# Performance work log

Hardware: AMD Instinct MI355X
Metric: run time of the kernel (lower is better)

## Reference

```python
import jax, jax.numpy as jnp
import numpy as np

N_NODES = 50000
N_EDGES = 600000
D = 128
N_LAYERS = 4  # 2 base + 2 resnet layers
N_GRAPHS = 64
NEG_SLOPE = 0.01  # F.leaky_relu default


def setup_inputs() -> dict:
    key = jax.random.key(0)
    k1, k2, k3, k4, k5 = jax.random.split(key, 5)
    x = jax.random.normal(k1, (N_NODES, D), dtype=jnp.float32)
    edge_index = jax.random.randint(k2, (2, N_EDGES), 0, N_NODES, dtype=jnp.int64)
    batch = jnp.sort(jax.random.randint(k3, (N_NODES,), 0, N_GRAPHS, dtype=jnp.int64))
    Wl = jax.random.normal(k4, (N_LAYERS, D, D), dtype=jnp.float32) * 0.05
    bl = jnp.zeros((N_LAYERS, D), dtype=jnp.float32)
    Wr = jax.random.normal(k5, (N_LAYERS, D, D), dtype=jnp.float32) * 0.05
    return {"x": x, "edge_index": edge_index, "batch": batch,
            "Wl": Wl, "bl": bl, "Wr": Wr}


def _mean_aggregate(x, src, dst, n_nodes):
    # mean over incoming neighbors; isolated nodes get 0 (PyG scatter-mean semantics)
    s = jax.ops.segment_sum(x[src], dst, num_segments=n_nodes)  # [N, D]
    cnt = jax.ops.segment_sum(jnp.ones((src.shape[0],), x.dtype), dst,
                              num_segments=n_nodes)
    return s / jnp.maximum(cnt, 1.0)[:, None]


def reference(x, edge_index, batch, Wl, bl, Wr):
    src, dst = edge_index[0], edge_index[1]
    n = x.shape[0]
    for i in range(N_LAYERS):
        agg = _mean_aggregate(x, src, dst, n)                      # [N, D]
        # SAGEConv: lin_l(agg) + lin_r(x); lin_l has bias, lin_r does not
        x_new = agg @ Wl[i].T + bl[i] + x @ Wr[i].T
        x_new = jnp.where(x_new >= 0, x_new, NEG_SLOPE * x_new)    # leaky_relu
        x = x_new if i < 2 else x + x_new                          # residual after first 2
    # global mean pool per graph
    pooled = jax.ops.segment_sum(x, batch, num_segments=N_GRAPHS)  # [G, D]
    counts = jax.ops.segment_sum(jnp.ones((n,), x.dtype), batch,
                                 num_segments=N_GRAPHS)
    return pooled / jnp.maximum(counts, 1.0)[:, None]
```

## Files before the change

kernel.cpp:

```cpp
#include <hip/hip_runtime.h>

#define N_NODES 50000
#define N_EDGES 600000
#define DIM 128
#define N_LAYERS 4
#define N_GRAPHS 64
#define NEG_SLOPE 0.01f
#define NB_SCAN ((N_NODES + 255) / 256)
#define RS 264

typedef __attribute__((ext_vector_type(8))) short short8;
typedef __attribute__((ext_vector_type(16))) float floatx16;

__device__ __forceinline__ unsigned short f2bf(float f) {
    union { float f; unsigned u; } c; c.f = f;
    unsigned u = c.u;
    unsigned r = (u + 0x7FFFu + ((u >> 16) & 1u)) >> 16;
    return (unsigned short)r;
}
__device__ __forceinline__ float bfraw2f(unsigned short b) {
    union { unsigned u; float f; } c; c.u = ((unsigned)b) << 16;
    return c.f;
}
__device__ __forceinline__ float bflo(unsigned u) {
    union { unsigned u; float f; } c; c.u = u << 16; return c.f;
}
__device__ __forceinline__ float bfhi(unsigned u) {
    union { unsigned u; float f; } c; c.u = u & 0xFFFF0000u; return c.f;
}


__global__ void zero_ints(int* p, int n) {
    int i = blockIdx.x * blockDim.x + threadIdx.x;
    if (i < n) p[i] = 0;
}

__global__ void convert_x(const float4* __restrict__ x, uint4* __restrict__ xb) {
    int i = blockIdx.x * blockDim.x + threadIdx.x;
    if (i >= N_NODES * DIM / 8) return;
    float4 a = x[i * 2], b = x[i * 2 + 1];
    uint4 o;
    o.x = ((unsigned)f2bf(a.y) << 16) | f2bf(a.x);
    o.y = ((unsigned)f2bf(a.w) << 16) | f2bf(a.z);
    o.z = ((unsigned)f2bf(b.y) << 16) | f2bf(b.x);
    o.w = ((unsigned)f2bf(b.w) << 16) | f2bf(b.z);
    xb[i] = o;
}

__global__ void pack_w(const float* __restrict__ Wl, const float* __restrict__ Wr,
                       ushort* __restrict__ wpk) {
    int s = blockIdx.x >> 2, t = blockIdx.x & 3;
    int m = blockIdx.y, layer = blockIdx.z;
    int l = threadIdx.x;
    const float* W = ((m == 0) ? Wl : Wr) + (size_t)layer * DIM * DIM;
    int n = t * 32 + (l & 31);
    int kb = s * 16 + (l >> 5) * 8;
    size_t off = ((((size_t)(layer * 2 + m) * 8 + s) * 4 + t) * 64 + l) * 8;
    for (int j = 0; j < 8; j++)
        wpk[off + j] = f2bf(W[n * DIM + kb + j]);
}

__global__ void count_deg(const int* __restrict__ dst, int* deg) {
    int e = blockIdx.x * blockDim.x + threadIdx.x;
    if (e < N_EDGES) atomicAdd(&deg[dst[e]], 1);
}

__global__ void scan_pass1(const int* __restrict__ deg, int* __restrict__ bsum) {
    int i = blockIdx.x * 256 + threadIdx.x;
    int v = (i < N_NODES) ? deg[i] : 0;
    for (int off = 32; off > 0; off >>= 1) v += __shfl_down(v, off, 64);
    __shared__ int ws[4];
    int lane = threadIdx.x & 63, w = threadIdx.x >> 6;
    if (lane == 0) ws[w] = v;
    __syncthreads();
    if (threadIdx.x == 0) bsum[blockIdx.x] = ws[0] + ws[1] + ws[2] + ws[3];
}

__global__ void scan_pass2(int* __restrict__ bsum) {
    __shared__ int sm[256];
    int t = threadIdx.x;
    int v = (t < NB_SCAN) ? bsum[t] : 0;
    sm[t] = v;
    __syncthreads();
    for (int off = 1; off < 256; off <<= 1) {
        int u = (t >= off) ? sm[t - off] : 0;
        __syncthreads();
        sm[t] += u;
        __syncthreads();
    }
    if (t < NB_SCAN) bsum[t] = sm[t] - v;
}

__global__ void scan_pass3(const int* __restrict__ deg, const int* __restrict__ bsum,
                           int* __restrict__ rp) {
    int i = blockIdx.x * 256 + threadIdx.x;
    int v = (i < N_NODES) ? deg[i] : 0;
    int lane = threadIdx.x & 63, w = threadIdx.x >> 6;
    int s = v;
    for (int off = 1; off < 64; off <<= 1) {
        int t = __shfl_up(s, off, 64);
        if (lane >= off) s += t;
    }
    __shared__ int ws[4];
    if (lane == 63) ws[w] = s;
    __syncthreads();
    int wo = 0;
    for (int k = 0; k < 4; k++) wo += (k < w) ? ws[k] : 0;
    int incl = s + wo + bsum[blockIdx.x];
    if (i < N_NODES) rp[i + 1] = incl;
    if (i == 0) rp[0] = 0;
}

__global__ void fill_csr(const int* __restrict__ src, const int* __restrict__ dst,
                         const int* __restrict__ rp, int* __restrict__ fill,
                         int* __restrict__ csr) {
    int e = blockIdx.x * blockDim.x + threadIdx.x;
    if (e >= N_EDGES) return;
    int d = dst[e];
    int pos = atomicAdd(&fill[d], 1);
    csr[rp[d] + pos] = src[e];
}

__global__ void graph_start(const int* __restrict__ batch, int* __restrict__ gstart) {
    int i = blockIdx.x * blockDim.x + threadIdx.x;
    if (i >= N_NODES) return;
    int b = batch[i];
    if (i == 0) {
        for (int g = 0; g <= b; g++) gstart[g] = 0;
    } else {
        int p = batch[i - 1];
        for (int g = p + 1; g <= b; g++) gstart[g] = i;
    }
    if (i == N_NODES - 1) {
        for (int g = b + 1; g <= N_GRAPHS; g++) gstart[g] = N_NODES;
    }
}

__global__ __launch_bounds__(256) void agg_mean_wave(const uint* __restrict__ x32,
                                                     const int* __restrict__ rp,
                                                     const int* __restrict__ csr,
                                                     uint* __restrict__ agg32) {
    int wv = threadIdx.x >> 6, lane = threadIdx.x & 63;
    int node = blockIdx.x * 4 + wv;
    if (node >= N_NODES) return;
    int s = rp[node], e = rp[node + 1];
    float a0 = 0.f, a1 = 0.f;
    for (int base = s; base < e; base += 64) {
        int cnt = min(64, e - base);
        unsigned myidx = (base + lane < e) ? (unsigned)csr[base + lane] : 0u;
        for (int j = 0; j < cnt; j += 8) {
            int c2 = min(8, cnt - j);
            unsigned v[8];
#pragma unroll
            for (int k = 0; k < 8; k++) {
                unsigned idx = __shfl(myidx, j + k, 64);
                v[k] = (k < c2) ? x32[(size_t)idx * 64 + lane] : 0u;
            }
#pragma unroll
            for (int k = 0; k < 8; k++) { a0 += bflo(v[k]); a1 += bfhi(v[k]); }
        }
    }
    float inv = 1.0f / (float)max(e - s, 1);
    unsigned o = ((unsigned)f2bf(a1 * inv) << 16) | f2bf(a0 * inv);
    agg32[(size_t)node * 64 + lane] = o;
}

__global__ __launch_bounds__(256) void fused_layer_mfma(const ushort* __restrict__ agg,
                                                        const ushort* __restrict__ xin,
                                                        ushort* __restrict__ xout,
                                                        const ushort* __restrict__ wpk,
                                                        const float* __restrict__ bias,
                                                        int residual) {
    __shared__ ushort sA[128 * RS];
    int t = threadIdx.x;
    int node0 = blockIdx.x * 128;

    const uint4* aggv = (const uint4*)(agg + (size_t)node0 * DIM);
    const uint4* xv   = (const uint4*)(xin + (size_t)node0 * DIM);
    for (int i = t; i < 128 * 32; i += 256) {
        int r = i >> 5, c = i & 31;
        uint4 val = make_uint4(0u, 0u, 0u, 0u);
        if (node0 + r < N_NODES)
            val = (c < 16) ? aggv[r * 16 + c] : xv[r * 16 + (c - 16)];
        *(uint4*)&sA[r * RS + c * 8] = val;
    }
    __syncthreads();

    int wv = t >> 6, l = t & 63;
    int m0 = wv * 32;
    const ushort* arow = &sA[(m0 + (l & 31)) * RS];
    int khalf = (l >> 5) * 8;

    floatx16 acc0, acc1, acc2, acc3;
    for (int ii = 0; ii < 16; ii++) acc0[ii] = acc1[ii] = acc2[ii] = acc3[ii] = 0.f;

    const ushort* wl8 = wpk + (size_t)l * 8;
#pragma unroll
    for (int s2 = 0; s2 < 16; s2++) {
        int m = s2 >> 3, s = s2 & 7;
        short8 a = *(const short8*)(arow + m * 128 + s * 16 + khalf);
        size_t fb = (size_t)((m * 8 + s) * 4) * 512;
        short8 b0 = *(const short8*)(wl8 + fb);
        short8 b1 = *(const short8*)(wl8 + fb + 512);
        short8 b2 = *(const short8*)(wl8 + fb + 1024);
        short8 b3 = *(const short8*)(wl8 + fb + 1536);
        acc0 = __builtin_amdgcn_mfma_f32_32x32x16_bf16(a, b0, acc0, 0, 0, 0);
        acc1 = __builtin_amdgcn_mfma_f32_32x32x16_bf16(a, b1, acc1, 0, 0, 0);
        acc2 = __builtin_amdgcn_mfma_f32_32x32x16_bf16(a, b2, acc2, 0, 0, 0);
        acc3 = __builtin_amdgcn_mfma_f32_32x32x16_bf16(a, b3, acc3, 0, 0, 0);
    }

    int col = l & 31;
    int rbase = 4 * (l >> 5);
    floatx16 accs[4] = {acc0, acc1, acc2, acc3};
    for (int t4 = 0; t4 < 4; t4++) {
        int n = t4 * 32 + col;
        float bv = bias[n];
#pragma unroll
        for (int r = 0; r < 16; r++) {
            int row = (r & 3) + 8 * (r >> 2) + rbase;
            int gm = m0 + row;
            int gn = node0 + gm;
            if (gn >= N_NODES) continue;
            float v = accs[t4][r] + bv;
            v = (v >= 0.f) ? v : NEG_SLOPE * v;
            if (residual) v += bfraw2f(sA[gm * RS + 128 + n]);
            xout[(size_t)gn * DIM + n] = f2bf(v);
        }
    }
}

__global__ __launch_bounds__(128) void pool_partial(const ushort* __restrict__ xb,
                                                    const int* __restrict__ batch,
                                                    float* __restrict__ pooled) {
    int nb = blockIdx.x * 128;
    int ne = min(nb + 128, N_NODES);
    int d = threadIdx.x;
    int gcur = batch[nb];
    float acc = 0.f;
    for (int n = nb; n < ne; n++) {
        int g = batch[n];
        if (g != gcur) {
            atomicAdd(&pooled[gcur * DIM + d], acc);
            acc = 0.f;
            gcur = g;
        }
        acc += bfraw2f(xb[(size_t)n * DIM + d]);
    }
    atomicAdd(&pooled[gcur * DIM + d], acc);
}

__global__ void pool_final(const float* __restrict__ pooled,
                           const int* __restrict__ gstart,
                           float* __restrict__ out) {
    int i = blockIdx.x * blockDim.x + threadIdx.x;
    if (i >= N_GRAPHS * DIM) return;
    int g = i >> 7;
    int cnt = gstart[g + 1] - gstart[g];
    out[i] = pooled[i] / (float)max(cnt, 1);
}


extern "C" void kernel_launch(void* const* d_in, const int* in_sizes, int n_in,
                              void* d_out, int out_size, void* d_ws, size_t ws_size,
                              hipStream_t stream) {
    const float* x     = (const float*)d_in[0];
    const int*   ei    = (const int*)d_in[1];
    const int*   batch = (const int*)d_in[2];
    const float* Wl    = (const float*)d_in[3];
    const float* bl    = (const float*)d_in[4];
    const float* Wr    = (const float*)d_in[5];
    float* out = (float*)d_out;

    const int* esrc = ei;
    const int* edst = ei + N_EDGES;

    ushort* xb0  = (ushort*)d_ws;
    ushort* xbuf = xb0 + (size_t)N_NODES * DIM;
    ushort* agg  = xbuf + (size_t)N_NODES * DIM;
    ushort* wpk  = agg + (size_t)N_NODES * DIM;
    int* deg    = (int*)(wpk + (size_t)N_LAYERS * 2 * DIM * DIM);
    int* fill   = deg + N_NODES;
    int* csr    = fill + N_NODES;
    int* rp     = csr + N_EDGES;
    int* gstart = rp + (N_NODES + 1);
    int* bsum   = gstart + (N_GRAPHS + 1);
    float* pooled = (float*)(bsum + NB_SCAN);

    zero_ints<<<(2 * N_NODES + 255) / 256, 256, 0, stream>>>(deg, 2 * N_NODES);
    zero_ints<<<(N_GRAPHS * DIM + 255) / 256, 256, 0, stream>>>((int*)pooled, N_GRAPHS * DIM);

    convert_x<<<(N_NODES * DIM / 8 + 255) / 256, 256, 0, stream>>>((const float4*)x, (uint4*)xb0);
    pack_w<<<dim3(32, 2, 4), 64, 0, stream>>>(Wl, Wr, wpk);
    count_deg<<<(N_EDGES + 255) / 256, 256, 0, stream>>>(edst, deg);

    scan_pass1<<<NB_SCAN, 256, 0, stream>>>(deg, bsum);
    scan_pass2<<<1, 256, 0, stream>>>(bsum);
    scan_pass3<<<NB_SCAN, 256, 0, stream>>>(deg, bsum, rp);

    fill_csr<<<(N_EDGES + 255) / 256, 256, 0, stream>>>(esrc, edst, rp, fill, csr);
    graph_start<<<(N_NODES + 255) / 256, 256, 0, stream>>>(batch, gstart);

    int agg_blocks = (N_NODES + 3) / 4;
    int gemm_blocks = (N_NODES + 127) / 128;
    for (int l = 0; l < N_LAYERS; l++) {
        const ushort* xin = (l == 0) ? xb0 : xbuf;
        agg_mean_wave<<<agg_blocks, 256, 0, stream>>>((const uint*)xin, rp, csr, (uint*)agg);
        fused_layer_mfma<<<gemm_blocks, 256, 0, stream>>>(
            agg, xin, xbuf, wpk + (size_t)l * 2 * DIM * DIM,
            bl + (size_t)l * DIM, (l >= 2) ? 1 : 0);
    }

    pool_partial<<<(N_NODES + 127) / 128, 128, 0, stream>>>(xbuf, batch, pooled);
    pool_final<<<(N_GRAPHS * DIM + 255) / 256, 256, 0, stream>>>(pooled, gstart, out);
}
```

Baseline: 375.0 us.

## Fuse neighbor mean aggregation into the per-layer MFMA GEMM kernel

The separate gather/mean kernel is merged into the layer kernel. Each wave now aggregates neighbors for its own 32 rows, two nodes at a time with 16-byte loads, and writes the bf16 means straight into shared memory before the MFMA GEMM. This removes the global write and re-read of the aggregation buffer and one launch per layer. Because neighbors are now read while outputs are written, the node features ping-pong between two buffers. The cost is that the latency-bound gather now runs on only a few hundred large-LDS blocks with few outstanding loads per wave, which may hide memory latency much worse than the old many-block gather kernel.

```diff
diff --git a/kernel.cpp b/kernel.cpp
--- a/kernel.cpp
+++ b/kernel.cpp
@@ -136,65 +136,92 @@
     }
 }
 
-__global__ __launch_bounds__(256) void agg_mean_wave(const uint* __restrict__ x32,
-                                                     const int* __restrict__ rp,
-                                                     const int* __restrict__ csr,
-                                                     uint* __restrict__ agg32) {
-    int wv = threadIdx.x >> 6, lane = threadIdx.x & 63;
-    int node = blockIdx.x * 4 + wv;
-    if (node >= N_NODES) return;
-    int s = rp[node], e = rp[node + 1];
-    float a0 = 0.f, a1 = 0.f;
-    for (int base = s; base < e; base += 64) {
-        int cnt = min(64, e - base);
-        unsigned myidx = (base + lane < e) ? (unsigned)csr[base + lane] : 0u;
-        for (int j = 0; j < cnt; j += 8) {
-            int c2 = min(8, cnt - j);
-            unsigned v[8];
-#pragma unroll
-            for (int k = 0; k < 8; k++) {
-                unsigned idx = __shfl(myidx, j + k, 64);
-                v[k] = (k < c2) ? x32[(size_t)idx * 64 + lane] : 0u;
-            }
-#pragma unroll
-            for (int k = 0; k < 8; k++) { a0 += bflo(v[k]); a1 += bfhi(v[k]); }
-        }
-    }
-    float inv = 1.0f / (float)max(e - s, 1);
-    unsigned o = ((unsigned)f2bf(a1 * inv) << 16) | f2bf(a0 * inv);
-    agg32[(size_t)node * 64 + lane] = o;
-}
-
-__global__ __launch_bounds__(256) void fused_layer_mfma(const ushort* __restrict__ agg,
-                                                        const ushort* __restrict__ xin,
-                                                        ushort* __restrict__ xout,
-                                                        const ushort* __restrict__ wpk,
-                                                        const float* __restrict__ bias,
-                                                        int residual) {
+__global__ __launch_bounds__(256) void sage_layer(const uint* __restrict__ x32,
+                                                  ushort* __restrict__ xout,
+                                                  const int* __restrict__ rp,
+                                                  const int* __restrict__ csr,
+                                                  const ushort* __restrict__ wpk,
+                                                  const float* __restrict__ bias,
+                                                  int residual) {
     __shared__ ushort sA[128 * RS];
     int t = threadIdx.x;
+    int wv = t >> 6, lane = t & 63;
     int node0 = blockIdx.x * 128;
-
-    const uint4* aggv = (const uint4*)(agg + (size_t)node0 * DIM);
-    const uint4* xv   = (const uint4*)(xin + (size_t)node0 * DIM);
-    for (int i = t; i < 128 * 32; i += 256) {
-        int r = i >> 5, c = i & 31;
-        uint4 val = make_uint4(0u, 0u, 0u, 0u);
-        if (node0 + r < N_NODES)
-            val = (c < 16) ? aggv[r * 16 + c] : xv[r * 16 + (c - 16)];
-        *(uint4*)&sA[r * RS + c * 8] = val;
-    }
-    __syncthreads();
-
-    int wv = t >> 6, l = t & 63;
     int m0 = wv * 32;
-    const ushort* arow = &sA[(m0 + (l & 31)) * RS];
-    int khalf = (l >> 5) * 8;
+    int ll = lane & 15, eg = lane >> 4;
+
+    const uint4* x16B = (const uint4*)x32;
+
+    for (int i = 0; i < 32; i += 2) {
+        int rA = m0 + i, rB = rA + 1;
+        int nA = node0 + rA, nB = node0 + rB;
+        int sAe = 0, eAe = 0, sBe = 0, eBe = 0;
+        if (nA < N_NODES) { sAe = rp[nA]; eAe = rp[nA + 1]; }
+        if (nB < N_NODES) { sBe = rp[nB]; eBe = rp[nB + 1]; }
+
+        unsigned xvA = (nA < N_NODES) ? x32[(size_t)nA * 64 + lane] : 0u;
+        unsigned xvB = (nB < N_NODES) ? x32[(size_t)nB * 64 + lane] : 0u;
+        ((uint*)(sA + (size_t)rA * RS))[64 + lane] = xvA;
+        ((uint*)(sA + (size_t)rB * RS))[64 + lane] = xvB;
+
+        float accA[8] = {0.f}, accB[8] = {0.f};
+        int baseA = sAe, baseB = sBe;
+        while (baseA < eAe || baseB < eBe) {
+            int cntA = (baseA < eAe) ? min(64, eAe - baseA) : 0;
+            int cntB = (baseB < eBe) ? min(64, eBe - baseB) : 0;
+            unsigned idxA = (baseA + lane < eAe) ? (unsigned)csr[baseA + lane] : 0u;
+            unsigned idxB = (baseB + lane < eBe) ? (unsigned)csr[baseB + lane] : 0u;
+            int mx = max(cntA, cntB);
+            for (int j = 0; j < mx; j += 4) {
+                int sel = j + eg;
+                unsigned iA = __shfl(idxA, sel & 63, 64);
+                unsigned iB = __shfl(idxB, sel & 63, 64);
+                uint4 vA = make_uint4(0u, 0u, 0u, 0u);
+                uint4 vB = make_uint4(0u, 0u, 0u, 0u);
+                if (sel < cntA) vA = x16B[(size_t)iA * 16 + ll];
+                if (sel < cntB) vB = x16B[(size_t)iB * 16 + ll];
+                accA[0] += bflo(vA.x); accA[1] += bfhi(vA.x);
+                accA[2] += bflo(vA.y); accA[3] += bfhi(vA.y);
+                accA[4] += bflo(vA.z); accA[5] += bfhi(vA.z);
+                accA[6] += bflo(vA.w); accA[7] += bfhi(vA.w);
+                accB[0] += bflo(vB.x); accB[1] += bfhi(vB.x);
+                accB[2] += bflo(vB.y); accB[3] += bfhi(vB.y);
+                accB[4] += bflo(vB.z); accB[5] += bfhi(vB.z);
+                accB[6] += bflo(vB.w); accB[7] += bfhi(vB.w);
+            }
+            baseA += 64; baseB += 64;
+        }
+#pragma unroll
+        for (int k = 0; k < 8; k++) {
+            accA[k] += __shfl_xor(accA[k], 16, 64);
+            accA[k] += __shfl_xor(accA[k], 32, 64);
+            accB[k] += __shfl_xor(accB[k], 16, 64);
+            accB[k] += __shfl_xor(accB[k], 32, 64);
+        }
+        float invA = 1.0f / (float)max(eAe - sAe, 1);
+        float invB = 1.0f / (float)max(eBe - sBe, 1);
+        if (eg == 0) {
+            uint4 oA, oB;
+            oA.x = ((unsigned)f2bf(accA[1] * invA) << 16) | f2bf(accA[0] * invA);
+            oA.y = ((unsigned)f2bf(accA[3] * invA) << 16) | f2bf(accA[2] * invA);
+            oA.z = ((unsigned)f2bf(accA[5] * invA) << 16) | f2bf(accA[4] * invA);
+            oA.w = ((unsigned)f2bf(accA[7] * invA) << 16) | f2bf(accA[6] * invA);
+            oB.x = ((unsigned)f2bf(accB[1] * invB) << 16) | f2bf(accB[0] * invB);
+            oB.y = ((unsigned)f2bf(accB[3] * invB) << 16) | f2bf(accB[2] * invB);
+            oB.z = ((unsigned)f2bf(accB[5] * invB) << 16) | f2bf(accB[4] * invB);
+            oB.w = ((unsigned)f2bf(accB[7] * invB) << 16) | f2bf(accB[6] * invB);
+            ((uint4*)(sA + (size_t)rA * RS))[ll] = oA;
+            ((uint4*)(sA + (size_t)rB * RS))[ll] = oB;
+        }
+    }
+
+    const ushort* arow = &sA[(size_t)(m0 + (lane & 31)) * RS];
+    int khalf = (lane >> 5) * 8;
 
     floatx16 acc0, acc1, acc2, acc3;
     for (int ii = 0; ii < 16; ii++) acc0[ii] = acc1[ii] = acc2[ii] = acc3[ii] = 0.f;
 
-    const ushort* wl8 = wpk + (size_t)l * 8;
+    const ushort* wl8 = wpk + (size_t)lane * 8;
 #pragma unroll
     for (int s2 = 0; s2 < 16; s2++) {
         int m = s2 >> 3, s = s2 & 7;
@@ -210,8 +237,8 @@
         acc3 = __builtin_amdgcn_mfma_f32_32x32x16_bf16(a, b3, acc3, 0, 0, 0);
     }
 
-    int col = l & 31;
-    int rbase = 4 * (l >> 5);
+    int col = lane & 31;
+    int rbase = 4 * (lane >> 5);
     floatx16 accs[4] = {acc0, acc1, acc2, acc3};
     for (int t4 = 0; t4 < 4; t4++) {
         int n = t4 * 32 + col;
@@ -224,7 +251,7 @@
             if (gn >= N_NODES) continue;
             float v = accs[t4][r] + bv;
             v = (v >= 0.f) ? v : NEG_SLOPE * v;
-            if (residual) v += bfraw2f(sA[gm * RS + 128 + n]);
+            if (residual) v += bfraw2f(sA[(size_t)gm * RS + 128 + n]);
             xout[(size_t)gn * DIM + n] = f2bf(v);
         }
     }
@@ -275,10 +302,10 @@
     const int* esrc = ei;
     const int* edst = ei + N_EDGES;
 
-    ushort* xb0  = (ushort*)d_ws;
-    ushort* xbuf = xb0 + (size_t)N_NODES * DIM;
-    ushort* agg  = xbuf + (size_t)N_NODES * DIM;
-    ushort* wpk  = agg + (size_t)N_NODES * DIM;
+    ushort* xb0 = (ushort*)d_ws;
+    ushort* xbA = xb0 + (size_t)N_NODES * DIM;
+    ushort* xbB = xbA + (size_t)N_NODES * DIM;
+    ushort* wpk = xbB + (size_t)N_NODES * DIM;
     int* deg    = (int*)(wpk + (size_t)N_LAYERS * 2 * DIM * DIM);
     int* fill   = deg + N_NODES;
     int* csr    = fill + N_NODES;
@@ -301,16 +328,17 @@
     fill_csr<<<(N_EDGES + 255) / 256, 256, 0, stream>>>(esrc, edst, rp, fill, csr);
     graph_start<<<(N_NODES + 255) / 256, 256, 0, stream>>>(batch, gstart);
 
-    int agg_blocks = (N_NODES + 3) / 4;
     int gemm_blocks = (N_NODES + 127) / 128;
+    const ushort* xin = xb0;
+    ushort* xo = xbA;
     for (int l = 0; l < N_LAYERS; l++) {
-        const ushort* xin = (l == 0) ? xb0 : xbuf;
-        agg_mean_wave<<<agg_blocks, 256, 0, stream>>>((const uint*)xin, rp, csr, (uint*)agg);
-        fused_layer_mfma<<<gemm_blocks, 256, 0, stream>>>(
-            agg, xin, xbuf, wpk + (size_t)l * 2 * DIM * DIM,
+        sage_layer<<<gemm_blocks, 256, 0, stream>>>(
+            (const uint*)xin, xo, rp, csr, wpk + (size_t)l * 2 * DIM * DIM,
             bl + (size_t)l * DIM, (l >= 2) ? 1 : 0);
-    }
-
-    pool_partial<<<(N_NODES + 127) / 128, 128, 0, stream>>>(xbuf, batch, pooled);
+        xin = xo;
+        xo = (xin == xbA) ? xbB : xbA;
+    }
+
+    pool_partial<<<(N_NODES + 127) / 128, 128, 0, stream>>>(xin, batch, pooled);
     pool_final<<<(N_GRAPHS * DIM + 255) / 256, 256, 0, stream>>>(pooled, gstart, out);
 }
```

Result: slower. 461.8 us (+23.2%).
